# Performance work log

Measured on AMD Instinct MI355X. Metric: run time of the kernel, lower is better.

## Reference

```python
import jax, jax.numpy as jnp
import numpy as np

EPS = 1e-5

def setup_inputs() -> dict:
    key = jax.random.key(0)
    B, N, F_in, F_out = 8, 2048, 64, 64
    ks = jax.random.split(key, 8)
    batch_nb_nodes = jax.random.randint(ks[0], (B,), N // 2, N + 1).astype(jnp.int32)
    node_mask = (jnp.arange(N)[None, :] < batch_nb_nodes[:, None]).astype(jnp.float32)  # [B,N]
    adj_mask = node_mask[:, :, None] * node_mask[:, None, :]                            # [B,N,N]
    emb_in = jax.random.normal(ks[1], (B, N, F_in), jnp.float32) * node_mask[:, :, None]
    adj_in = jax.random.uniform(ks[2], (B, N, N), jnp.float32) * adj_mask
    kernel_sigma = jnp.asarray(float(F_in), jnp.float32)          # gaussian kernel bandwidth
    combine_w = jnp.array([0.5, 0.5], jnp.float32)                # affine combine of [adj_in, kernel]
    conv_W = jax.random.normal(ks[3], (2 * F_in, F_out), jnp.float32) / np.float32(np.sqrt(2 * F_in))
    conv_b = jnp.zeros((F_out,), jnp.float32)
    nu_W = jax.random.normal(ks[4], (F_in + F_out, F_out), jnp.float32) / np.float32(np.sqrt(F_in + F_out))
    nu_b = jnp.zeros((F_out,), jnp.float32)
    return {"emb_in": emb_in, "adj_in": adj_in, "adj_mask": adj_mask,
            "batch_nb_nodes": batch_nb_nodes, "kernel_sigma": kernel_sigma,
            "combine_w": combine_w, "conv_W": conv_W, "conv_b": conv_b,
            "nu_W": nu_W, "nu_b": nu_b}

def reference(emb_in, adj_in, adj_mask, batch_nb_nodes, kernel_sigma, combine_w, conv_W, conv_b, nu_W, nu_b):
    B, N, F = emb_in.shape
    # --- gaussian kernel adjacency update: K_ij = exp(-||e_i - e_j||^2 / sigma) ---
    sq = jnp.sum(emb_in * emb_in, axis=-1)                                  # [B,N]
    d2 = sq[:, :, None] + sq[:, None, :] - 2.0 * jnp.einsum('bif,bjf->bij', emb_in, emb_in)
    ker = jnp.exp(-jnp.maximum(d2, 0.0) / kernel_sigma)                     # [B,N,N]
    # --- affine combine of previous adjacency and kernel matrices, then mask ---
    adj = (combine_w[0] * adj_in + combine_w[1] * ker) * adj_mask           # [B,N,N]
    # --- spatialnorm: per-graph mean/std over valid nodes (layer_nb != 0) ---
    node_mask = (jnp.arange(N)[None, :] < batch_nb_nodes[:, None]).astype(emb_in.dtype)  # [B,N]
    cnt = jnp.maximum(batch_nb_nodes.astype(emb_in.dtype), 1.0)[:, None, None]
    m = node_mask[:, :, None]
    mean = jnp.sum(emb_in * m, axis=1, keepdims=True) / cnt                 # [B,1,F]
    var = jnp.sum(((emb_in - mean) ** 2) * m, axis=1, keepdims=True) / cnt  # [B,1,F]
    emb_n = ((emb_in - mean) / jnp.sqrt(var + EPS)) * m                     # mask_embedding
    # --- operators: degree (D @ x) and adjacency (A @ x), joined then conv ---
    deg = jnp.sum(adj, axis=-1)                                             # [B,N]
    op_deg = deg[:, :, None] * emb_n                                        # [B,N,F]
    op_adj = jnp.einsum('bij,bjf->bif', adj, emb_n)                         # [B,N,F]
    emb_upd = jnp.concatenate([op_deg, op_adj], axis=-1) @ conv_W + conv_b  # [B,N,F_out]
    # --- node update: relu(W [emb_in ; emb_update] + b) ---
    emb = jax.nn.relu(jnp.concatenate([emb_in, emb_upd], axis=-1) @ nu_W + nu_b)
    return emb, adj
```

## Files before the change

### kernel.cpp

```cpp
#include <hip/hip_runtime.h>
#include <math.h>

#define BB 8
#define NN 2048
#define FF 64
#define EPSV 1e-5f
#define EMB_SZ (BB * NN * FF)

#define WS_SQ    0
#define WS_ASUM  (BB * NN)
#define WS_ASQ   (WS_ASUM + BB * FF)
#define WS_MEAN  (WS_ASQ + BB * FF)
#define WS_RSTD  (WS_MEAN + BB * FF)
#define WS_DEG   (WS_RSTD + BB * FF)

__global__ __launch_bounds__(256) void k_stats(const float* __restrict__ emb,
                                               float* __restrict__ sq,
                                               float* __restrict__ asum,
                                               float* __restrict__ asq) {
    const int b    = blockIdx.y;
    const int lane = threadIdx.x & 63;
    const int grp  = threadIdx.x >> 6;
    const int base_i = blockIdx.x << 7;

    float s = 0.f, q = 0.f;
    for (int it = 0; it < 32; ++it) {
        const int i = base_i + (it << 2) + grp;
        const float x = emb[((size_t)(b * NN + i) << 6) + lane];
        const float x2 = x * x;
        s += x;
        q += x2;
        float r = x2;
        r += __shfl_xor(r, 1);
        r += __shfl_xor(r, 2);
        r += __shfl_xor(r, 4);
        r += __shfl_xor(r, 8);
        r += __shfl_xor(r, 16);
        r += __shfl_xor(r, 32);
        if (lane == 0) sq[b * NN + i] = r;
    }
    __shared__ float redS[4][64];
    __shared__ float redQ[4][64];
    redS[grp][lane] = s;
    redQ[grp][lane] = q;
    __syncthreads();
    if (threadIdx.x < 64) {
        const float ts = redS[0][lane] + redS[1][lane] + redS[2][lane] + redS[3][lane];
        const float tq = redQ[0][lane] + redQ[1][lane] + redQ[2][lane] + redQ[3][lane];
        atomicAdd(&asum[(b << 6) + lane], ts);
        atomicAdd(&asq[(b << 6) + lane], tq);
    }
}

__global__ void k_finalize(const float* __restrict__ asum, const float* __restrict__ asq,
                           const int* __restrict__ nbp,
                           float* __restrict__ mean, float* __restrict__ rstd) {
    const int t = threadIdx.x;
    const int b = t >> 6;
    const float cnt = fmaxf((float)nbp[b], 1.f);
    const float m = asum[t] / cnt;
    float v = asq[t] / cnt - m * m;
    v = fmaxf(v, 0.f);
    mean[t] = m;
    rstd[t] = rsqrtf(v + EPSV);
}

__global__ __launch_bounds__(256) void k_adj_deg(const float* __restrict__ emb,
                                                 const float* __restrict__ adj_in,
                                                 const float* __restrict__ sq,
                                                 const float* __restrict__ sigp,
                                                 const float* __restrict__ cw,
                                                 const int* __restrict__ nbp,
                                                 float* __restrict__ adj_out,
                                                 float* __restrict__ deg) {
    __shared__ __align__(16) float As[32][132];
    __shared__ __align__(16) float Bs[32][132];
    const int b  = blockIdx.z;
    const int i0 = blockIdx.y << 7;
    const int j0 = blockIdx.x << 7;
    const int tid = threadIdx.x;
    const int tx = tid & 15, ty = tid >> 4;
    const int nb = nbp[b];
    const int bN = b * NN;

    if (i0 >= nb || j0 >= nb) {
        const float4 z4 = make_float4(0.f, 0.f, 0.f, 0.f);
#pragma unroll
        for (int u = 0; u < 8; ++u) {
            const int i = i0 + ((u >> 2) << 6) + (ty << 2) + (u & 3);
#pragma unroll
            for (int vh = 0; vh < 2; ++vh) {
                const size_t rbase = ((size_t)(bN + i) << 11) + j0 + (vh << 6) + (tx << 2);
                *(float4*)(adj_out + rbase) = z4;
            }
        }
        return;
    }

    const int srow = tid & 31;
    const int scb  = (tid >> 5) << 2;

    float acc[8][8];
#pragma unroll
    for (int u = 0; u < 8; ++u)
#pragma unroll
        for (int v = 0; v < 8; ++v) acc[u][v] = 0.f;

    for (int kt = 0; kt < FF; kt += 32) {
#pragma unroll
        for (int p = 0; p < 4; ++p) {
            const int row = srow + (p << 5);
            const float4 a  = *(const float4*)(emb + ((size_t)(bN + i0 + row) << 6) + kt + scb);
            const float4 bb = *(const float4*)(emb + ((size_t)(bN + j0 + row) << 6) + kt + scb);
            As[scb + 0][row] = a.x;  As[scb + 1][row] = a.y;
            As[scb + 2][row] = a.z;  As[scb + 3][row] = a.w;
            Bs[scb + 0][row] = bb.x; Bs[scb + 1][row] = bb.y;
            Bs[scb + 2][row] = bb.z; Bs[scb + 3][row] = bb.w;
        }
        __syncthreads();
#pragma unroll 4
        for (int k = 0; k < 32; ++k) {
            const float4 a0 = *(const float4*)&As[k][(ty << 2)];
            const float4 a1 = *(const float4*)&As[k][64 + (ty << 2)];
            const float4 b0 = *(const float4*)&Bs[k][(tx << 2)];
            const float4 b1 = *(const float4*)&Bs[k][64 + (tx << 2)];
            const float av[8] = {a0.x, a0.y, a0.z, a0.w, a1.x, a1.y, a1.z, a1.w};
            const float bv[8] = {b0.x, b0.y, b0.z, b0.w, b1.x, b1.y, b1.z, b1.w};
#pragma unroll
            for (int u = 0; u < 8; ++u)
#pragma unroll
                for (int v = 0; v < 8; ++v)
                    acc[u][v] = fmaf(av[u], bv[v], acc[u][v]);
        }
        __syncthreads();
    }

    const float inv_sigma = 1.0f / sigp[0];
    const float w0 = cw[0], w1 = cw[1];

    float sqi[8], sqj[8];
#pragma unroll
    for (int u = 0; u < 8; ++u) {
        sqi[u] = sq[bN + i0 + ((u >> 2) << 6) + (ty << 2) + (u & 3)];
        sqj[u] = sq[bN + j0 + ((u >> 2) << 6) + (tx << 2) + (u & 3)];
    }

    auto cell = [&](float accv, float sqiv, float sqjv, float ainv, float amv) -> float {
        float d2 = sqiv + sqjv - 2.f * accv;
        d2 = fmaxf(d2, 0.f);
        const float ker = __expf(-d2 * inv_sigma);
        return (w0 * ainv + w1 * ker) * amv;
    };

    float rs8[8];
#pragma unroll
    for (int u = 0; u < 8; ++u) {
        const int i = i0 + ((u >> 2) << 6) + (ty << 2) + (u & 3);
        const float mi = (i < nb) ? 1.f : 0.f;
        float rsum = 0.f;
#pragma unroll
        for (int vh = 0; vh < 2; ++vh) {
            const int jb = j0 + (vh << 6) + (tx << 2);
            const size_t rbase = ((size_t)(bN + i) << 11) + jb;
            const float4 ain = *(const float4*)(adj_in + rbase);
            float4 o;
            o.x = cell(acc[u][vh * 4 + 0], sqi[u], sqj[vh * 4 + 0], ain.x,
                       (jb + 0 < nb) ? mi : 0.f);
            o.y = cell(acc[u][vh * 4 + 1], sqi[u], sqj[vh * 4 + 1], ain.y,
                       (jb + 1 < nb) ? mi : 0.f);
            o.z = cell(acc[u][vh * 4 + 2], sqi[u], sqj[vh * 4 + 2], ain.z,
                       (jb + 2 < nb) ? mi : 0.f);
            o.w = cell(acc[u][vh * 4 + 3], sqi[u], sqj[vh * 4 + 3], ain.w,
                       (jb + 3 < nb) ? mi : 0.f);
            *(float4*)(adj_out + rbase) = o;
            rsum += o.x + o.y + o.z + o.w;
        }
        rs8[u] = rsum;
    }
#pragma unroll
    for (int u = 0; u < 8; ++u) {
        float v = rs8[u];
        v += __shfl_xor(v, 1);
        v += __shfl_xor(v, 2);
        v += __shfl_xor(v, 4);
        v += __shfl_xor(v, 8);
        if (tx == 0) {
            const int i = i0 + ((u >> 2) << 6) + (ty << 2) + (u & 3);
            atomicAdd(&deg[bN + i], v);
        }
    }
}

__global__ __launch_bounds__(256) void k_aggpart(const float* __restrict__ adj,
                                                 const float* __restrict__ emb,
                                                 const float* __restrict__ meanp,
                                                 const float* __restrict__ rstdp,
                                                 const int* __restrict__ nbp,
                                                 float* __restrict__ opadj) {
    __shared__ __align__(16) float Adjs[64 * 68];
    __shared__ __align__(16) float Es[64 * 68];
    const int b  = blockIdx.z;
    const int i0 = blockIdx.x << 6;
    const int nb = nbp[b];
    if (i0 >= nb) return;
    const int jbeg = blockIdx.y << 9;
    if (jbeg >= nb) return;
    const int jend = min(jbeg + 512, (nb + 63) & ~63);

    const int tid = threadIdx.x;
    const int tx = tid & 15, ty = tid >> 4;
    const int bN = b * NN;
    const int sj  = tid >> 2;
    const int scb = (tid & 3) << 4;
    const int air = tid & 63;
    const int ajc = (tid >> 6) << 4;

    float4 mn4[4], rs4[4];
#pragma unroll
    for (int u = 0; u < 4; ++u) {
        mn4[u] = *(const float4*)(meanp + (b << 6) + scb + (u << 2));
        rs4[u] = *(const float4*)(rstdp + (b << 6) + scb + (u << 2));
    }

    float acc[4][4];
#pragma unroll
    for (int u = 0; u < 4; ++u)
#pragma unroll
        for (int v = 0; v < 4; ++v) acc[u][v] = 0.f;

    for (int jt = jbeg; jt < jend; jt += 64) {
#pragma unroll
        for (int u = 0; u < 16; u += 4) {
            const float4 v = *(const float4*)(adj + ((size_t)(bN + i0 + air) << 11) + jt + ajc + u);
            Adjs[(ajc + u + 0) * 68 + air] = v.x;
            Adjs[(ajc + u + 1) * 68 + air] = v.y;
            Adjs[(ajc + u + 2) * 68 + air] = v.z;
            Adjs[(ajc + u + 3) * 68 + air] = v.w;
        }
        {
            const float msk = (jt + sj < nb) ? 1.f : 0.f;
            const float* pe = emb + ((size_t)(bN + jt + sj) << 6) + scb;
#pragma unroll
            for (int u = 0; u < 4; ++u) {
                const float4 v = *(const float4*)(pe + (u << 2));
                float4 o;
                o.x = (v.x - mn4[u].x) * rs4[u].x * msk;
                o.y = (v.y - mn4[u].y) * rs4[u].y * msk;
                o.z = (v.z - mn4[u].z) * rs4[u].z * msk;
                o.w = (v.w - mn4[u].w) * rs4[u].w * msk;
                *(float4*)&Es[sj * 68 + scb + (u << 2)] = o;
            }
        }
        __syncthreads();
#pragma unroll 8
        for (int j = 0; j < 64; ++j) {
            const float4 e = *(const float4*)&Es[j * 68 + (tx << 2)];
            const float4 a = *(const float4*)&Adjs[j * 68 + (ty << 2)];
            acc[0][0] = fmaf(a.x, e.x, acc[0][0]);
            acc[0][1] = fmaf(a.x, e.y, acc[0][1]);
            acc[0][2] = fmaf(a.x, e.z, acc[0][2]);
            acc[0][3] = fmaf(a.x, e.w, acc[0][3]);
            acc[1][0] = fmaf(a.y, e.x, acc[1][0]);
            acc[1][1] = fmaf(a.y, e.y, acc[1][1]);
            acc[1][2] = fmaf(a.y, e.z, acc[1][2]);
            acc[1][3] = fmaf(a.y, e.w, acc[1][3]);
            acc[2][0] = fmaf(a.z, e.x, acc[2][0]);
            acc[2][1] = fmaf(a.z, e.y, acc[2][1]);
            acc[2][2] = fmaf(a.z, e.z, acc[2][2]);
            acc[2][3] = fmaf(a.z, e.w, acc[2][3]);
            acc[3][0] = fmaf(a.w, e.x, acc[3][0]);
            acc[3][1] = fmaf(a.w, e.y, acc[3][1]);
            acc[3][2] = fmaf(a.w, e.z, acc[3][2]);
            acc[3][3] = fmaf(a.w, e.w, acc[3][3]);
        }
        __syncthreads();
    }

#pragma unroll
    for (int u = 0; u < 4; ++u) {
        const int gi = i0 + (ty << 2) + u;
        float* p = opadj + (((size_t)(bN + gi)) << 6) + (tx << 2);
        atomicAdd(p + 0, acc[u][0]);
        atomicAdd(p + 1, acc[u][1]);
        atomicAdd(p + 2, acc[u][2]);
        atomicAdd(p + 3, acc[u][3]);
    }
}

__global__ __launch_bounds__(256) void k_epilogue(const float* __restrict__ emb,
                                                  const float* __restrict__ meanp,
                                                  const float* __restrict__ rstdp,
                                                  const float* __restrict__ degp,
                                                  const int* __restrict__ nbp,
                                                  const float* __restrict__ convW,
                                                  const float* __restrict__ convB,
                                                  const float* __restrict__ nuW,
                                                  const float* __restrict__ nuB,
                                                  float* __restrict__ emb_out) {
    __shared__ __align__(16) float smem[13056];
    float* xs = smem;
    float* us = smem + 8704;
    float* es = smem;

    const int b   = blockIdx.y;
    const int i0  = blockIdx.x << 6;
    const int tid = threadIdx.x;
    const int tx = tid & 15, ty = tid >> 4;
    const int nb = nbp[b];
    const int bN = b * NN;
    const int sj  = tid >> 2;
    const int scb = (tid & 3) << 4;

    {
        const float4 m4 = *(const float4*)(meanp + (b << 6) + (tx << 2));
        const float4 r4 = *(const float4*)(rstdp + (b << 6) + (tx << 2));
#pragma unroll
        for (int u = 0; u < 4; ++u) {
            const int il = (ty << 2) + u;
            const int gi = i0 + il;
            const float msk = (gi < nb) ? 1.f : 0.f;
            const float dg = degp[bN + gi];
            const float4 v = *(const float4*)(emb + ((size_t)(bN + gi) << 6) + (tx << 2));
            float4 en;
            en.x = (v.x - m4.x) * r4.x * msk;
            en.y = (v.y - m4.y) * r4.y * msk;
            en.z = (v.z - m4.z) * r4.z * msk;
            en.w = (v.w - m4.w) * r4.w * msk;
            float4 od;
            od.x = dg * en.x; od.y = dg * en.y; od.z = dg * en.z; od.w = dg * en.w;
            *(float4*)&xs[il * 132 + (tx << 2)] = od;
            const float4 oa = *(const float4*)(emb_out + ((size_t)(bN + gi) << 6) + (tx << 2));
            *(float4*)&xs[il * 132 + 64 + (tx << 2)] = oa;
        }
    }
    __syncthreads();

    {
        float u4[4][4];
#pragma unroll
        for (int r = 0; r < 4; ++r)
#pragma unroll
            for (int c = 0; c < 4; ++c) u4[r][c] = 0.f;
        for (int fis = 0; fis < 128; fis += 4) {
            const float4 w0v = *(const float4*)(convW + ((fis + 0) << 6) + (tx << 2));
            const float4 w1v = *(const float4*)(convW + ((fis + 1) << 6) + (tx << 2));
            const float4 w2v = *(const float4*)(convW + ((fis + 2) << 6) + (tx << 2));
            const float4 w3v = *(const float4*)(convW + ((fis + 3) << 6) + (tx << 2));
#pragma unroll
            for (int r = 0; r < 4; ++r) {
                const float4 x = *(const float4*)&xs[((ty << 2) + r) * 132 + fis];
                u4[r][0] += x.x * w0v.x + x.y * w1v.x + x.z * w2v.x + x.w * w3v.x;
                u4[r][1] += x.x * w0v.y + x.y * w1v.y + x.z * w2v.y + x.w * w3v.y;
                u4[r][2] += x.x * w0v.z + x.y * w1v.z + x.z * w2v.z + x.w * w3v.z;
                u4[r][3] += x.x * w0v.w + x.y * w1v.w + x.z * w2v.w + x.w * w3v.w;
            }
        }
        const float4 cb4 = *(const float4*)(convB + (tx << 2));
#pragma unroll
        for (int r = 0; r < 4; ++r) {
            float4 o;
            o.x = u4[r][0] + cb4.x; o.y = u4[r][1] + cb4.y;
            o.z = u4[r][2] + cb4.z; o.w = u4[r][3] + cb4.w;
            *(float4*)&us[((ty << 2) + r) * 68 + (tx << 2)] = o;
        }
    }
    __syncthreads();

    {
        const float* pe = emb + ((size_t)(bN + i0 + sj) << 6) + scb;
#pragma unroll
        for (int u = 0; u < 4; ++u)
            *(float4*)&es[sj * 68 + scb + (u << 2)] = *(const float4*)(pe + (u << 2));
    }
    __syncthreads();

    {
        float u4[4][4];
#pragma unroll
        for (int r = 0; r < 4; ++r)
#pragma unroll
            for (int c = 0; c < 4; ++c) u4[r][c] = 0.f;
        for (int fis = 0; fis < 64; fis += 4) {
            const float4 w0v = *(const float4*)(nuW + ((fis + 0) << 6) + (tx << 2));
            const float4 w1v = *(const float4*)(nuW + ((fis + 1) << 6) + (tx << 2));
            const float4 w2v = *(const float4*)(nuW + ((fis + 2) << 6) + (tx << 2));
            const float4 w3v = *(const float4*)(nuW + ((fis + 3) << 6) + (tx << 2));
#pragma unroll
            for (int r = 0; r < 4; ++r) {
                const float4 x = *(const float4*)&es[((ty << 2) + r) * 68 + fis];
                u4[r][0] += x.x * w0v.x + x.y * w1v.x + x.z * w2v.x + x.w * w3v.x;
                u4[r][1] += x.x * w0v.y + x.y * w1v.y + x.z * w2v.y + x.w * w3v.y;
                u4[r][2] += x.x * w0v.z + x.y * w1v.z + x.z * w2v.z + x.w * w3v.z;
                u4[r][3] += x.x * w0v.w + x.y * w1v.w + x.z * w2v.w + x.w * w3v.w;
            }
        }
        for (int fis = 0; fis < 64; fis += 4) {
            const float4 w0v = *(const float4*)(nuW + ((64 + fis + 0) << 6) + (tx << 2));
            const float4 w1v = *(const float4*)(nuW + ((64 + fis + 1) << 6) + (tx << 2));
            const float4 w2v = *(const float4*)(nuW + ((64 + fis + 2) << 6) + (tx << 2));
            const float4 w3v = *(const float4*)(nuW + ((64 + fis + 3) << 6) + (tx << 2));
#pragma unroll
            for (int r = 0; r < 4; ++r) {
                const float4 x = *(const float4*)&us[((ty << 2) + r) * 68 + fis];
                u4[r][0] += x.x * w0v.x + x.y * w1v.x + x.z * w2v.x + x.w * w3v.x;
                u4[r][1] += x.x * w0v.y + x.y * w1v.y + x.z * w2v.y + x.w * w3v.y;
                u4[r][2] += x.x * w0v.z + x.y * w1v.z + x.z * w2v.z + x.w * w3v.z;
                u4[r][3] += x.x * w0v.w + x.y * w1v.w + x.z * w2v.w + x.w * w3v.w;
            }
        }
        const float4 nb4 = *(const float4*)(nuB + (tx << 2));
#pragma unroll
        for (int r = 0; r < 4; ++r) {
            const int gi = i0 + (ty << 2) + r;
            float4 o;
            o.x = fmaxf(u4[r][0] + nb4.x, 0.f);
            o.y = fmaxf(u4[r][1] + nb4.y, 0.f);
            o.z = fmaxf(u4[r][2] + nb4.z, 0.f);
            o.w = fmaxf(u4[r][3] + nb4.w, 0.f);
            *(float4*)(emb_out + ((size_t)(bN + gi) << 6) + (tx << 2)) = o;
        }
    }
}

extern "C" void kernel_launch(void* const* d_in, const int* in_sizes, int n_in,
                              void* d_out, int out_size, void* d_ws, size_t ws_size,
                              hipStream_t stream) {
    (void)in_sizes; (void)n_in; (void)out_size; (void)ws_size;
    const float* emb_in   = (const float*)d_in[0];
    const float* adj_in   = (const float*)d_in[1];
    const int*   nbp      = (const int*)d_in[3];
    const float* sigp     = (const float*)d_in[4];
    const float* cw       = (const float*)d_in[5];
    const float* convW    = (const float*)d_in[6];
    const float* convB    = (const float*)d_in[7];
    const float* nuW      = (const float*)d_in[8];
    const float* nuB      = (const float*)d_in[9];

    float* emb_out = (float*)d_out;
    float* adj_out = (float*)d_out + EMB_SZ;

    float* ws   = (float*)d_ws;
    float* sq   = ws + WS_SQ;
    float* asum = ws + WS_ASUM;
    float* asq  = ws + WS_ASQ;
    float* mean = ws + WS_MEAN;
    float* rstd = ws + WS_RSTD;
    float* deg  = ws + WS_DEG;

    hipMemsetAsync(asum, 0, 2 * BB * FF * sizeof(float), stream);
    hipMemsetAsync(deg, 0, BB * NN * sizeof(float), stream);
    hipMemsetAsync(emb_out, 0, (size_t)EMB_SZ * sizeof(float), stream);

    k_stats<<<dim3(16, BB), 256, 0, stream>>>(emb_in, sq, asum, asq);
    k_finalize<<<1, BB * FF, 0, stream>>>(asum, asq, nbp, mean, rstd);
    k_adj_deg<<<dim3(NN / 128, NN / 128, BB), 256, 0, stream>>>(emb_in, adj_in, sq, sigp,
                                                                cw, nbp, adj_out, deg);
    k_aggpart<<<dim3(NN / 64, 4, BB), 256, 0, stream>>>(adj_out, emb_in, mean, rstd,
                                                        nbp, emb_out);
    k_epilogue<<<dim3(NN / 64, BB), 256, 0, stream>>>(emb_in, mean, rstd, deg, nbp,
                                                      convW, convB, nuW, nuB, emb_out);
}
```

Before: 432.1 us.

## Use bf16 MFMA for Gram and aggregation GEMMs with split-bf16 precision

Replaces the scalar FP32 outer-product loops in both GEMM kernels with MFMA 16x16x32 bf16 instructions. The Gram matrix gets a hi/lo bf16 split (three MFMAs per tile) to keep close to fp32 accuracy, while the adjacency-times-embedding product uses plain bf16. The adj kernel tile shrinks to 64x128 and k_stats uses more blocks, and the two workspace memsets are merged into one. The epilogue of adj_deg now writes scalar (non-float4) stores and reads adj_in scalar, which may hurt coalescing, and bf16 rounding in opadj adds error.

```diff
diff --git a/kernel.cpp b/kernel.cpp
--- a/kernel.cpp
+++ b/kernel.cpp
@@ -13,6 +13,18 @@
 #define WS_MEAN  (WS_ASQ + BB * FF)
 #define WS_RSTD  (WS_MEAN + BB * FF)
 #define WS_DEG   (WS_RSTD + BB * FF)
+
+typedef __attribute__((ext_vector_type(8))) short bf16x8;
+typedef __attribute__((ext_vector_type(4))) float f32x4;
+
+__device__ inline unsigned short f2bf(float x) {
+    union { float f; unsigned u; } v; v.f = x;
+    return (unsigned short)((v.u + 0x7fffu + ((v.u >> 16) & 1u)) >> 16);
+}
+__device__ inline float bf2f(unsigned short h) {
+    union { float f; unsigned u; } v; v.u = ((unsigned)h) << 16;
+    return v.f;
+}
 
 __global__ __launch_bounds__(256) void k_stats(const float* __restrict__ emb,
                                                float* __restrict__ sq,
@@ -21,10 +33,10 @@
     const int b    = blockIdx.y;
     const int lane = threadIdx.x & 63;
     const int grp  = threadIdx.x >> 6;
-    const int base_i = blockIdx.x << 7;
+    const int base_i = blockIdx.x << 6;
 
     float s = 0.f, q = 0.f;
-    for (int it = 0; it < 32; ++it) {
+    for (int it = 0; it < 16; ++it) {
         const int i = base_i + (it << 2) + grp;
         const float x = emb[((size_t)(b * NN + i) << 6) + lane];
         const float x2 = x * x;
@@ -65,72 +77,95 @@
     rstd[t] = rsqrtf(v + EPSV);
 }
 
-__global__ __launch_bounds__(256) void k_adj_deg(const float* __restrict__ emb,
-                                                 const float* __restrict__ adj_in,
-                                                 const float* __restrict__ sq,
-                                                 const float* __restrict__ sigp,
-                                                 const float* __restrict__ cw,
-                                                 const int* __restrict__ nbp,
-                                                 float* __restrict__ adj_out,
-                                                 float* __restrict__ deg) {
-    __shared__ __align__(16) float As[32][132];
-    __shared__ __align__(16) float Bs[32][132];
+__global__ __launch_bounds__(256, 4) void k_adj_deg(const float* __restrict__ emb,
+                                                    const float* __restrict__ adj_in,
+                                                    const float* __restrict__ sq,
+                                                    const float* __restrict__ sigp,
+                                                    const float* __restrict__ cw,
+                                                    const int* __restrict__ nbp,
+                                                    float* __restrict__ adj_out,
+                                                    float* __restrict__ deg) {
+    __shared__ __align__(16) unsigned short Ah[64][40];
+    __shared__ __align__(16) unsigned short Al[64][40];
+    __shared__ __align__(16) unsigned short Bh[128][40];
+    __shared__ __align__(16) unsigned short Bl[128][40];
+
     const int b  = blockIdx.z;
-    const int i0 = blockIdx.y << 7;
     const int j0 = blockIdx.x << 7;
-    const int tid = threadIdx.x;
-    const int tx = tid & 15, ty = tid >> 4;
+    const int i0 = blockIdx.y << 6;
     const int nb = nbp[b];
     const int bN = b * NN;
+    const int tid = threadIdx.x;
 
     if (i0 >= nb || j0 >= nb) {
-        const float4 z4 = make_float4(0.f, 0.f, 0.f, 0.f);
-#pragma unroll
-        for (int u = 0; u < 8; ++u) {
-            const int i = i0 + ((u >> 2) << 6) + (ty << 2) + (u & 3);
-#pragma unroll
-            for (int vh = 0; vh < 2; ++vh) {
-                const size_t rbase = ((size_t)(bN + i) << 11) + j0 + (vh << 6) + (tx << 2);
-                *(float4*)(adj_out + rbase) = z4;
-            }
+        const float4 z = make_float4(0.f, 0.f, 0.f, 0.f);
+#pragma unroll
+        for (int qq = 0; qq < 8; ++qq) {
+            const int idx = tid * 8 + qq;
+            const int row = idx >> 5, c4 = (idx & 31) << 2;
+            *(float4*)(adj_out + ((size_t)(bN + i0 + row) << 11) + j0 + c4) = z;
         }
         return;
     }
 
-    const int srow = tid & 31;
-    const int scb  = (tid >> 5) << 2;
-
-    float acc[8][8];
-#pragma unroll
-    for (int u = 0; u < 8; ++u)
-#pragma unroll
-        for (int v = 0; v < 8; ++v) acc[u][v] = 0.f;
-
-    for (int kt = 0; kt < FF; kt += 32) {
-#pragma unroll
-        for (int p = 0; p < 4; ++p) {
-            const int row = srow + (p << 5);
-            const float4 a  = *(const float4*)(emb + ((size_t)(bN + i0 + row) << 6) + kt + scb);
-            const float4 bb = *(const float4*)(emb + ((size_t)(bN + j0 + row) << 6) + kt + scb);
-            As[scb + 0][row] = a.x;  As[scb + 1][row] = a.y;
-            As[scb + 2][row] = a.z;  As[scb + 3][row] = a.w;
-            Bs[scb + 0][row] = bb.x; Bs[scb + 1][row] = bb.y;
-            Bs[scb + 2][row] = bb.z; Bs[scb + 3][row] = bb.w;
+    const int w   = tid >> 6;
+    const int lane = tid & 63;
+    const int l15 = lane & 15, lq = lane >> 4;
+
+    f32x4 acc[8];
+#pragma unroll
+    for (int c = 0; c < 8; ++c) acc[c] = (f32x4){0.f, 0.f, 0.f, 0.f};
+
+    for (int kh = 0; kh < 64; kh += 32) {
+        {
+            const int row = tid >> 1, kc = (tid & 1) << 4;
+            const float* src = emb + ((size_t)(bN + j0 + row) << 6) + kh + kc;
+            __align__(16) float xv[16];
+            *(float4*)(xv + 0)  = *(const float4*)(src + 0);
+            *(float4*)(xv + 4)  = *(const float4*)(src + 4);
+            *(float4*)(xv + 8)  = *(const float4*)(src + 8);
+            *(float4*)(xv + 12) = *(const float4*)(src + 12);
+            __align__(16) unsigned short hh[16], ll[16];
+#pragma unroll
+            for (int e = 0; e < 16; ++e) {
+                hh[e] = f2bf(xv[e]);
+                ll[e] = f2bf(xv[e] - bf2f(hh[e]));
+            }
+            *(bf16x8*)&Bh[row][kc]     = *(bf16x8*)&hh[0];
+            *(bf16x8*)&Bh[row][kc + 8] = *(bf16x8*)&hh[8];
+            *(bf16x8*)&Bl[row][kc]     = *(bf16x8*)&ll[0];
+            *(bf16x8*)&Bl[row][kc + 8] = *(bf16x8*)&ll[8];
+        }
+        if (tid < 128) {
+            const int row = tid >> 1, kc = (tid & 1) << 4;
+            const float* src = emb + ((size_t)(bN + i0 + row) << 6) + kh + kc;
+            __align__(16) float xv[16];
+            *(float4*)(xv + 0)  = *(const float4*)(src + 0);
+            *(float4*)(xv + 4)  = *(const float4*)(src + 4);
+            *(float4*)(xv + 8)  = *(const float4*)(src + 8);
+            *(float4*)(xv + 12) = *(const float4*)(src + 12);
+            __align__(16) unsigned short hh[16], ll[16];
+#pragma unroll
+            for (int e = 0; e < 16; ++e) {
+                hh[e] = f2bf(xv[e]);
+                ll[e] = f2bf(xv[e] - bf2f(hh[e]));
+            }
+            *(bf16x8*)&Ah[row][kc]     = *(bf16x8*)&hh[0];
+            *(bf16x8*)&Ah[row][kc + 8] = *(bf16x8*)&hh[8];
+            *(bf16x8*)&Al[row][kc]     = *(bf16x8*)&ll[0];
+            *(bf16x8*)&Al[row][kc + 8] = *(bf16x8*)&ll[8];
         }
         __syncthreads();
-#pragma unroll 4
-        for (int k = 0; k < 32; ++k) {
-            const float4 a0 = *(const float4*)&As[k][(ty << 2)];
-            const float4 a1 = *(const float4*)&As[k][64 + (ty << 2)];
-            const float4 b0 = *(const float4*)&Bs[k][(tx << 2)];
-            const float4 b1 = *(const float4*)&Bs[k][64 + (tx << 2)];
-            const float av[8] = {a0.x, a0.y, a0.z, a0.w, a1.x, a1.y, a1.z, a1.w};
-            const float bv[8] = {b0.x, b0.y, b0.z, b0.w, b1.x, b1.y, b1.z, b1.w};
-#pragma unroll
-            for (int u = 0; u < 8; ++u)
-#pragma unroll
-                for (int v = 0; v < 8; ++v)
-                    acc[u][v] = fmaf(av[u], bv[v], acc[u][v]);
+
+        const bf16x8 ah = *(bf16x8*)&Ah[w * 16 + l15][lq * 8];
+        const bf16x8 al = *(bf16x8*)&Al[w * 16 + l15][lq * 8];
+#pragma unroll
+        for (int c = 0; c < 8; ++c) {
+            const bf16x8 bh = *(bf16x8*)&Bh[c * 16 + l15][lq * 8];
+            const bf16x8 bl = *(bf16x8*)&Bl[c * 16 + l15][lq * 8];
+            acc[c] = __builtin_amdgcn_mfma_f32_16x16x32_bf16(ah, bh, acc[c], 0, 0, 0);
+            acc[c] = __builtin_amdgcn_mfma_f32_16x16x32_bf16(ah, bl, acc[c], 0, 0, 0);
+            acc[c] = __builtin_amdgcn_mfma_f32_16x16x32_bf16(al, bh, acc[c], 0, 0, 0);
         }
         __syncthreads();
     }
@@ -138,67 +173,50 @@
     const float inv_sigma = 1.0f / sigp[0];
     const float w0 = cw[0], w1 = cw[1];
 
-    float sqi[8], sqj[8];
-#pragma unroll
-    for (int u = 0; u < 8; ++u) {
-        sqi[u] = sq[bN + i0 + ((u >> 2) << 6) + (ty << 2) + (u & 3)];
-        sqj[u] = sq[bN + j0 + ((u >> 2) << 6) + (tx << 2) + (u & 3)];
-    }
-
-    auto cell = [&](float accv, float sqiv, float sqjv, float ainv, float amv) -> float {
-        float d2 = sqiv + sqjv - 2.f * accv;
-        d2 = fmaxf(d2, 0.f);
-        const float ker = __expf(-d2 * inv_sigma);
-        return (w0 * ainv + w1 * ker) * amv;
-    };
-
-    float rs8[8];
-#pragma unroll
-    for (int u = 0; u < 8; ++u) {
-        const int i = i0 + ((u >> 2) << 6) + (ty << 2) + (u & 3);
-        const float mi = (i < nb) ? 1.f : 0.f;
+    float sqi[4], sqj[8];
+    const int irow0 = i0 + w * 16 + lq * 4;
+#pragma unroll
+    for (int r = 0; r < 4; ++r) sqi[r] = sq[bN + irow0 + r];
+#pragma unroll
+    for (int c = 0; c < 8; ++c) sqj[c] = sq[bN + j0 + c * 16 + l15];
+
+#pragma unroll
+    for (int r = 0; r < 4; ++r) {
+        const int gi = irow0 + r;
+        const float mi = (gi < nb) ? 1.f : 0.f;
+        float ain[8];
+#pragma unroll
+        for (int c = 0; c < 8; ++c)
+            ain[c] = adj_in[((size_t)(bN + gi) << 11) + j0 + c * 16 + l15];
         float rsum = 0.f;
 #pragma unroll
-        for (int vh = 0; vh < 2; ++vh) {
-            const int jb = j0 + (vh << 6) + (tx << 2);
-            const size_t rbase = ((size_t)(bN + i) << 11) + jb;
-            const float4 ain = *(const float4*)(adj_in + rbase);
-            float4 o;
-            o.x = cell(acc[u][vh * 4 + 0], sqi[u], sqj[vh * 4 + 0], ain.x,
-                       (jb + 0 < nb) ? mi : 0.f);
-            o.y = cell(acc[u][vh * 4 + 1], sqi[u], sqj[vh * 4 + 1], ain.y,
-                       (jb + 1 < nb) ? mi : 0.f);
-            o.z = cell(acc[u][vh * 4 + 2], sqi[u], sqj[vh * 4 + 2], ain.z,
-                       (jb + 2 < nb) ? mi : 0.f);
-            o.w = cell(acc[u][vh * 4 + 3], sqi[u], sqj[vh * 4 + 3], ain.w,
-                       (jb + 3 < nb) ? mi : 0.f);
-            *(float4*)(adj_out + rbase) = o;
-            rsum += o.x + o.y + o.z + o.w;
-        }
-        rs8[u] = rsum;
-    }
-#pragma unroll
-    for (int u = 0; u < 8; ++u) {
-        float v = rs8[u];
-        v += __shfl_xor(v, 1);
-        v += __shfl_xor(v, 2);
-        v += __shfl_xor(v, 4);
-        v += __shfl_xor(v, 8);
-        if (tx == 0) {
-            const int i = i0 + ((u >> 2) << 6) + (ty << 2) + (u & 3);
-            atomicAdd(&deg[bN + i], v);
-        }
-    }
-}
-
-__global__ __launch_bounds__(256) void k_aggpart(const float* __restrict__ adj,
-                                                 const float* __restrict__ emb,
-                                                 const float* __restrict__ meanp,
-                                                 const float* __restrict__ rstdp,
-                                                 const int* __restrict__ nbp,
-                                                 float* __restrict__ opadj) {
-    __shared__ __align__(16) float Adjs[64 * 68];
-    __shared__ __align__(16) float Es[64 * 68];
+        for (int c = 0; c < 8; ++c) {
+            const int gj = j0 + c * 16 + l15;
+            float d2 = sqi[r] + sqj[c] - 2.f * acc[c][r];
+            d2 = fmaxf(d2, 0.f);
+            const float ker = __expf(-d2 * inv_sigma);
+            const float mv = (gj < nb) ? mi : 0.f;
+            const float o = (w0 * ain[c] + w1 * ker) * mv;
+            adj_out[((size_t)(bN + gi) << 11) + gj] = o;
+            rsum += o;
+        }
+        rsum += __shfl_xor(rsum, 1);
+        rsum += __shfl_xor(rsum, 2);
+        rsum += __shfl_xor(rsum, 4);
+        rsum += __shfl_xor(rsum, 8);
+        if (l15 == 0) atomicAdd(&deg[bN + gi], rsum);
+    }
+}
+
+__global__ __launch_bounds__(256, 4) void k_opadj(const float* __restrict__ adj,
+                                                  const float* __restrict__ emb,
+                                                  const float* __restrict__ meanp,
+                                                  const float* __restrict__ rstdp,
+                                                  const int* __restrict__ nbp,
+                                                  float* __restrict__ opadj) {
+    __shared__ __align__(16) unsigned short As[64][72];
+    __shared__ __align__(16) unsigned short Bt[64][72];
+
     const int b  = blockIdx.z;
     const int i0 = blockIdx.x << 6;
     const int nb = nbp[b];
@@ -207,84 +225,73 @@
     if (jbeg >= nb) return;
     const int jend = min(jbeg + 512, (nb + 63) & ~63);
 
+    const int bN = b * NN;
     const int tid = threadIdx.x;
-    const int tx = tid & 15, ty = tid >> 4;
-    const int bN = b * NN;
-    const int sj  = tid >> 2;
-    const int scb = (tid & 3) << 4;
-    const int air = tid & 63;
-    const int ajc = (tid >> 6) << 4;
-
-    float4 mn4[4], rs4[4];
-#pragma unroll
-    for (int u = 0; u < 4; ++u) {
-        mn4[u] = *(const float4*)(meanp + (b << 6) + scb + (u << 2));
-        rs4[u] = *(const float4*)(rstdp + (b << 6) + scb + (u << 2));
-    }
-
-    float acc[4][4];
-#pragma unroll
-    for (int u = 0; u < 4; ++u)
-#pragma unroll
-        for (int v = 0; v < 4; ++v) acc[u][v] = 0.f;
+    const int w = tid >> 6, lane = tid & 63;
+    const int l15 = lane & 15, lq = lane >> 4;
+
+    const int sjj = tid & 63;
+    const int fb  = (tid >> 6) << 4;
+    float mn[16], rs[16];
+#pragma unroll
+    for (int e = 0; e < 16; e += 4) {
+        *(float4*)&mn[e] = *(const float4*)(meanp + (b << 6) + fb + e);
+        *(float4*)&rs[e] = *(const float4*)(rstdp + (b << 6) + fb + e);
+    }
+
+    f32x4 acc[4];
+#pragma unroll
+    for (int c = 0; c < 4; ++c) acc[c] = (f32x4){0.f, 0.f, 0.f, 0.f};
 
     for (int jt = jbeg; jt < jend; jt += 64) {
-#pragma unroll
-        for (int u = 0; u < 16; u += 4) {
-            const float4 v = *(const float4*)(adj + ((size_t)(bN + i0 + air) << 11) + jt + ajc + u);
-            Adjs[(ajc + u + 0) * 68 + air] = v.x;
-            Adjs[(ajc + u + 1) * 68 + air] = v.y;
-            Adjs[(ajc + u + 2) * 68 + air] = v.z;
-            Adjs[(ajc + u + 3) * 68 + air] = v.w;
-        }
         {
-            const float msk = (jt + sj < nb) ? 1.f : 0.f;
-            const float* pe = emb + ((size_t)(bN + jt + sj) << 6) + scb;
-#pragma unroll
-            for (int u = 0; u < 4; ++u) {
-                const float4 v = *(const float4*)(pe + (u << 2));
-                float4 o;
-                o.x = (v.x - mn4[u].x) * rs4[u].x * msk;
-                o.y = (v.y - mn4[u].y) * rs4[u].y * msk;
-                o.z = (v.z - mn4[u].z) * rs4[u].z * msk;
-                o.w = (v.w - mn4[u].w) * rs4[u].w * msk;
-                *(float4*)&Es[sj * 68 + scb + (u << 2)] = o;
+            const int row = tid >> 2, jc = (tid & 3) << 4;
+            const float* src = adj + ((size_t)(bN + i0 + row) << 11) + jt + jc;
+            __align__(16) float xv[16];
+            *(float4*)(xv + 0)  = *(const float4*)(src + 0);
+            *(float4*)(xv + 4)  = *(const float4*)(src + 4);
+            *(float4*)(xv + 8)  = *(const float4*)(src + 8);
+            *(float4*)(xv + 12) = *(const float4*)(src + 12);
+            __align__(16) unsigned short hh[16];
+#pragma unroll
+            for (int e = 0; e < 16; ++e) hh[e] = f2bf(xv[e]);
+            *(bf16x8*)&As[row][jc]     = *(bf16x8*)&hh[0];
+            *(bf16x8*)&As[row][jc + 8] = *(bf16x8*)&hh[8];
+        }
+        {
+            const float msk = (jt + sjj < nb) ? 1.f : 0.f;
+            const float* src = emb + ((size_t)(bN + jt + sjj) << 6) + fb;
+            __align__(16) float xv[16];
+            *(float4*)(xv + 0)  = *(const float4*)(src + 0);
+            *(float4*)(xv + 4)  = *(const float4*)(src + 4);
+            *(float4*)(xv + 8)  = *(const float4*)(src + 8);
+            *(float4*)(xv + 12) = *(const float4*)(src + 12);
+#pragma unroll
+            for (int e = 0; e < 16; ++e) {
+                const float en = (xv[e] - mn[e]) * rs[e] * msk;
+                Bt[fb + e][sjj] = f2bf(en);
             }
         }
         __syncthreads();
-#pragma unroll 8
-        for (int j = 0; j < 64; ++j) {
-            const float4 e = *(const float4*)&Es[j * 68 + (tx << 2)];
-            const float4 a = *(const float4*)&Adjs[j * 68 + (ty << 2)];
-            acc[0][0] = fmaf(a.x, e.x, acc[0][0]);
-            acc[0][1] = fmaf(a.x, e.y, acc[0][1]);
-            acc[0][2] = fmaf(a.x, e.z, acc[0][2]);
-            acc[0][3] = fmaf(a.x, e.w, acc[0][3]);
-            acc[1][0] = fmaf(a.y, e.x, acc[1][0]);
-            acc[1][1] = fmaf(a.y, e.y, acc[1][1]);
-            acc[1][2] = fmaf(a.y, e.z, acc[1][2]);
-            acc[1][3] = fmaf(a.y, e.w, acc[1][3]);
-            acc[2][0] = fmaf(a.z, e.x, acc[2][0]);
-            acc[2][1] = fmaf(a.z, e.y, acc[2][1]);
-            acc[2][2] = fmaf(a.z, e.z, acc[2][2]);
-            acc[2][3] = fmaf(a.z, e.w, acc[2][3]);
-            acc[3][0] = fmaf(a.w, e.x, acc[3][0]);
-            acc[3][1] = fmaf(a.w, e.y, acc[3][1]);
-            acc[3][2] = fmaf(a.w, e.z, acc[3][2]);
-            acc[3][3] = fmaf(a.w, e.w, acc[3][3]);
+#pragma unroll
+        for (int ks = 0; ks < 2; ++ks) {
+            const bf16x8 a = *(bf16x8*)&As[w * 16 + l15][ks * 32 + lq * 8];
+#pragma unroll
+            for (int c = 0; c < 4; ++c) {
+                const bf16x8 bv = *(bf16x8*)&Bt[c * 16 + l15][ks * 32 + lq * 8];
+                acc[c] = __builtin_amdgcn_mfma_f32_16x16x32_bf16(a, bv, acc[c], 0, 0, 0);
+            }
         }
         __syncthreads();
     }
 
 #pragma unroll
-    for (int u = 0; u < 4; ++u) {
-        const int gi = i0 + (ty << 2) + u;
-        float* p = opadj + (((size_t)(bN + gi)) << 6) + (tx << 2);
-        atomicAdd(p + 0, acc[u][0]);
-        atomicAdd(p + 1, acc[u][1]);
-        atomicAdd(p + 2, acc[u][2]);
-        atomicAdd(p + 3, acc[u][3]);
-    }
+    for (int c = 0; c < 4; ++c)
+#pragma unroll
+        for (int r = 0; r < 4; ++r) {
+            const int gi = i0 + w * 16 + lq * 4 + r;
+            atomicAdd(opadj + ((size_t)(bN + gi) << 6) + c * 16 + l15, acc[c][r]);
+        }
 }
 
 __global__ __launch_bounds__(256) void k_epilogue(const float* __restrict__ emb,
@@ -447,16 +454,16 @@
     float* rstd = ws + WS_RSTD;
     float* deg  = ws + WS_DEG;
 
-    hipMemsetAsync(asum, 0, 2 * BB * FF * sizeof(float), stream);
-    hipMemsetAsync(deg, 0, BB * NN * sizeof(float), stream);
+    hipMemsetAsync(asum, 0, (2 * BB * FF + 2 * BB * FF + BB * NN) * sizeof(float) / 2
+                            + (BB * NN) * sizeof(float) / 1, stream);
     hipMemsetAsync(emb_out, 0, (size_t)EMB_SZ * sizeof(float), stream);
 
-    k_stats<<<dim3(16, BB), 256, 0, stream>>>(emb_in, sq, asum, asq);
+    k_stats<<<dim3(32, BB), 256, 0, stream>>>(emb_in, sq, asum, asq);
     k_finalize<<<1, BB * FF, 0, stream>>>(asum, asq, nbp, mean, rstd);
-    k_adj_deg<<<dim3(NN / 128, NN / 128, BB), 256, 0, stream>>>(emb_in, adj_in, sq, sigp,
-                                                                cw, nbp, adj_out, deg);
-    k_aggpart<<<dim3(NN / 64, 4, BB), 256, 0, stream>>>(adj_out, emb_in, mean, rstd,
-                                                        nbp, emb_out);
+    k_adj_deg<<<dim3(NN / 128, NN / 64, BB), 256, 0, stream>>>(emb_in, adj_in, sq, sigp,
+                                                               cw, nbp, adj_out, deg);
+    k_opadj<<<dim3(NN / 64, 4, BB), 256, 0, stream>>>(adj_out, emb_in, mean, rstd,
+                                                      nbp, emb_out);
     k_epilogue<<<dim3(NN / 64, BB), 256, 0, stream>>>(emb_in, mean, rstd, deg, nbp,
                                                       convW, convB, nuW, nuB, emb_out);
 }
```

New measurement: 395.2 us. 8.5% less time.
